# Kernel optimization log

Hardware: AMD Instinct MI355X
Metric: run time of the kernel (lower is better)

The kernel has to match this reference:

```python
import jax, jax.numpy as jnp
import numpy as np

SEQ_LEN = 4096
EMBED_DIM = 1024
NUM_HEADS = 16  # head_dim = 64


def setup_inputs() -> dict:
    key = jax.random.key(0)
    k0, k1, k2 = jax.random.split(key, 3)
    std = 0.02
    x = jax.random.normal(k0, (SEQ_LEN, EMBED_DIM), dtype=jnp.float32)
    # torch Linear convention: weight [out_features, in_features], y = x @ W.T + b
    W_qkv = jax.random.normal(k1, (3 * EMBED_DIM, EMBED_DIM), dtype=jnp.float32) * std
    b_qkv = jnp.zeros((3 * EMBED_DIM,), dtype=jnp.float32)
    W_out = jax.random.normal(k2, (EMBED_DIM, EMBED_DIM), dtype=jnp.float32) * std
    b_out = jnp.zeros((EMBED_DIM,), dtype=jnp.float32)
    return {"input": x, "W_qkv": W_qkv, "b_qkv": b_qkv, "W_out": W_out, "b_out": b_out}


def reference(input, W_qkv, b_qkv, W_out, b_out):
    S, E = input.shape
    H = NUM_HEADS
    Dh = E // H
    # fused QKV projection: [S, 3E]
    projected = input @ W_qkv.T + b_qkv
    q, k, v = jnp.split(projected, 3, axis=1)          # each [S, E]
    q = q.reshape(S, H, Dh)
    k = k.reshape(S, H, Dh)
    v = v.reshape(S, H, Dh)
    # unscaled attention (the original applies no 1/sqrt(d) scaling)
    scores = jnp.einsum('shd,thd->hst', q, k)          # [H, S, S] -- full matrix in HBM
    probs = jax.nn.softmax(scores, axis=-1)
    out = jnp.einsum('hst,thd->shd', probs, v)         # [S, H, Dh]
    out = out.reshape(S, E)
    return out @ W_out.T + b_out
```

## Files before the change

### kernel.cpp

```cpp
#include <hip/hip_runtime.h>

typedef unsigned short u16;
typedef short    bf16x8 __attribute__((ext_vector_type(8)));
typedef u16      u16x8  __attribute__((ext_vector_type(8)));
typedef u16      u16x4  __attribute__((ext_vector_type(4)));
typedef float    f32x4  __attribute__((ext_vector_type(4)));
typedef unsigned u32x2  __attribute__((ext_vector_type(2)));

__device__ __forceinline__ u16 f2bf(float f) {
  unsigned x = __float_as_uint(f);
  unsigned r = x + 0x7fffu + ((x >> 16) & 1u);
  return (u16)(r >> 16);
}
__device__ __forceinline__ float bf2f(u16 u) {
  return __uint_as_float(((unsigned)u) << 16);
}
__device__ __forceinline__ float exp2v(float x) {
  float r;
  asm("v_exp_f32 %0, %1" : "=v"(r) : "v"(x));
  return r;
}

__global__ __launch_bounds__(256) void cast_bf16(const float* __restrict__ src,
                                                 u16* __restrict__ dst) {
  int i = blockIdx.x * 256 + threadIdx.x;
  f32x4 v = ((const f32x4*)src)[i];
  u16x4 o;
  o[0] = f2bf(v[0]); o[1] = f2bf(v[1]); o[2] = f2bf(v[2]); o[3] = f2bf(v[3]);
  ((u16x4*)dst)[i] = o;
}

template<int N, int K, bool OUTF32, bool SCALEQ>
__global__ __launch_bounds__(256) void gemm_bt(const u16* __restrict__ A,
                                               const u16* __restrict__ B,
                                               const float* __restrict__ bias,
                                               void* __restrict__ Cout) {
  __shared__ __align__(16) u16 As[2][128 * 32];
  __shared__ __align__(16) u16 Bs[2][128 * 32];
  const int tid = threadIdx.x;
  const int flat = blockIdx.y * gridDim.x + blockIdx.x;
  const int q8 = (gridDim.x * gridDim.y) >> 3;
  const int sw = (flat & 7) * q8 + (flat >> 3);
  const int m0 = (sw / gridDim.x) * 128, n0 = (sw % gridDim.x) * 128;
  const int wave = tid >> 6, lane = tid & 63;
  const int c = lane & 15, g = lane >> 4;
  const int wm = (wave >> 1) * 64, wn = (wave & 1) * 64;
  f32x4 acc[4][4] = {};

  const int sr = wave * 16 + (lane >> 2);
  const int sc = (lane & 3) * 8;

  auto stage = [&](int buf, int k0) {
#pragma unroll
    for (int j = 0; j < 2; j++) {
      __builtin_amdgcn_global_load_lds(
        (const __attribute__((address_space(1))) void*)(A + (size_t)(m0 + j * 64 + sr) * K + k0 + sc),
        (__attribute__((address_space(3))) void*)&As[buf][(j * 64 + wave * 16) * 32], 16, 0, 0);
      __builtin_amdgcn_global_load_lds(
        (const __attribute__((address_space(1))) void*)(B + (size_t)(n0 + j * 64 + sr) * K + k0 + sc),
        (__attribute__((address_space(3))) void*)&Bs[buf][(j * 64 + wave * 16) * 32], 16, 0, 0);
    }
  };

  stage(0, 0);
  __syncthreads();

  const int nT = K / 32;
  for (int t = 0; t < nT; ++t) {
    const int buf = t & 1;
    if (t + 1 < nT) stage(buf ^ 1, (t + 1) * 32);
    bf16x8 af[4], bfr[4];
#pragma unroll
    for (int m = 0; m < 4; m++) af[m]  = *(const bf16x8*)&As[buf][(wm + m * 16 + c) * 32 + g * 8];
#pragma unroll
    for (int n = 0; n < 4; n++) bfr[n] = *(const bf16x8*)&Bs[buf][(wn + n * 16 + c) * 32 + g * 8];
#pragma unroll
    for (int m = 0; m < 4; m++)
#pragma unroll
      for (int n = 0; n < 4; n++)
        acc[m][n] = __builtin_amdgcn_mfma_f32_16x16x32_bf16(af[m], bfr[n], acc[m][n], 0, 0, 0);
    __syncthreads();
  }

  const float qscale = (SCALEQ && n0 < 1024) ? 1.44269504f : 1.0f;
#pragma unroll
  for (int n = 0; n < 4; n++) {
    float bv = bias[n0 + wn + n * 16 + c];
#pragma unroll
    for (int m = 0; m < 4; m++) {
#pragma unroll
      for (int r = 0; r < 4; r++) {
        float val = (acc[m][n][r] + bv) * qscale;
        int row = m0 + wm + m * 16 + g * 4 + r;
        int col = n0 + wn + n * 16 + c;
        if constexpr (OUTF32) ((float*)Cout)[(size_t)row * N + col] = val;
        else                  ((u16*)Cout)[(size_t)row * N + col] = f2bf(val);
      }
    }
  }
}

__global__ __launch_bounds__(256) void transpose_v(const u16* __restrict__ qkv,
                                                   u16* __restrict__ vt) {
  __shared__ u16 tile[64][64];
  int h  = blockIdx.x >> 6;
  int s0 = (blockIdx.x & 63) * 64;
  int t = threadIdx.x;
  int row = t >> 3, ch = t & 7;
#pragma unroll
  for (int rep = 0; rep < 2; rep++) {
    int r = rep * 32 + row;
    u16x8 v = *(const u16x8*)&qkv[(size_t)(s0 + r) * 3072 + 2048 + h * 64 + ch * 8];
    *(u16x8*)&tile[r][ch * 8] = v;
  }
  __syncthreads();
#pragma unroll
  for (int rep = 0; rep < 2; rep++) {
    int d = rep * 32 + row;
    u16x8 w;
#pragma unroll
    for (int j = 0; j < 8; j++) w[j] = tile[ch * 8 + j][d];
    *(u16x8*)&vt[(size_t)(h * 64 + d) * 4096 + s0 + ch * 8] = w;
  }
}

__global__ __launch_bounds__(256, 4) void attn_kernel(const u16* __restrict__ qkv,
                                                      const u16* __restrict__ vt,
                                                      u16* __restrict__ pb0,
                                                      u16* __restrict__ pb1,
                                                      float* __restrict__ lb0,
                                                      float* __restrict__ lb1) {
  const int bid = blockIdx.x;
  const int kk  = bid & 1;
  const int qt  = (bid >> 1) & 31;
  const int h   = bid >> 6;
  const int q0  = qt * 128;
  const int kbase = kk * 2048;
  const int tid = threadIdx.x;
  const int wave = tid >> 6, lane = tid & 63;
  const int c = lane & 15, g = lane >> 4;
  const int qw = q0 + wave * 32;

  __shared__ __align__(16) u16 kls[2][64 * 64];
  __shared__ __align__(16) u16 vls[2][64 * 64];
  __shared__ __align__(16) unsigned plds[4][16 * 32];
  unsigned* pw = plds[wave];
  const int pswz = (c & 7) << 2;

  const u16* Kg = qkv + 1024 + h * 64;
  const u16* Vg = vt + (size_t)h * 64 * 4096;

  const int srow = lane >> 3, sgr = lane & 7;
  const int gc = sgr ^ (srow & 7);
  const u16* kp = Kg + (size_t)(kbase + wave * 16 + srow) * 3072 + gc * 8;
  const u16* vp = Vg + (size_t)(wave * 16 + srow) * 4096 + kbase + gc * 8;

  auto stage = [&](int buf, const u16* kpp, const u16* vpp) {
#pragma unroll
    for (int j = 0; j < 2; j++) {
      __builtin_amdgcn_global_load_lds(
        (const __attribute__((address_space(1))) void*)(kpp + (size_t)j * 8 * 3072),
        (__attribute__((address_space(3))) void*)&kls[buf][(wave * 16 + j * 8) * 64], 16, 0, 0);
      __builtin_amdgcn_global_load_lds(
        (const __attribute__((address_space(1))) void*)(vpp + (size_t)j * 8 * 4096),
        (__attribute__((address_space(3))) void*)&vls[buf][(wave * 16 + j * 8) * 64], 16, 0, 0);
    }
  };

  bf16x8 qf[2][2];
#pragma unroll
  for (int qs = 0; qs < 2; qs++)
#pragma unroll
    for (int dc = 0; dc < 2; dc++)
      qf[qs][dc] = *(const bf16x8*)&qkv[(size_t)(qw + qs * 16 + c) * 3072 + h * 64 + dc * 32 + g * 8];

  bf16x8 ones;
#pragma unroll
  for (int j = 0; j < 8; j++) ones[j] = (short)0x3F80;

  f32x4 o0[4] = {}, o1[4] = {};
  f32x4 accl0 = {}, accl1 = {};
  const f32x4 minit = {-16.f, -16.f, -16.f, -16.f};

  auto softmax = [&](f32x4 (&st)[4]) {
#pragma unroll
    for (int ks = 0; ks < 4; ks++) {
      float p0 = exp2v(st[ks][0]), p1 = exp2v(st[ks][1]);
      float p2 = exp2v(st[ks][2]), p3 = exp2v(st[ks][3]);
      unsigned w0, w1;
      asm("v_cvt_pk_bf16_f32 %0, %1, %2" : "=v"(w0) : "v"(p0), "v"(p1));
      asm("v_cvt_pk_bf16_f32 %0, %1, %2" : "=v"(w1) : "v"(p2), "v"(p3));
      u32x2 w2 = {w0, w1};
      *(u32x2*)&pw[c * 32 + ((ks * 8 + g * 2) ^ pswz)] = w2;
    }
  };

  stage(0, kp, vp);
  kp += (size_t)64 * 3072; vp += 64;
  __syncthreads();

  for (int t = 0; t < 32; ++t) {
    const int buf = t & 1;
    if (t + 1 < 32) {
      stage(buf ^ 1, kp, vp);
      kp += (size_t)64 * 3072; vp += 64;
    }

    f32x4 st0[4], st1[4];
    __builtin_amdgcn_s_setprio(1);
#pragma unroll
    for (int ks = 0; ks < 4; ks++) {
      bf16x8 kf0 = *(const bf16x8*)&kls[buf][(ks * 16 + c) * 64 + ((g ^ (c & 7)) << 3)];
      bf16x8 kf1 = *(const bf16x8*)&kls[buf][(ks * 16 + c) * 64 + (((4 + g) ^ (c & 7)) << 3)];
      f32x4 s0 = __builtin_amdgcn_mfma_f32_16x16x32_bf16(kf0, qf[0][0], minit, 0, 0, 0);
      st0[ks]  = __builtin_amdgcn_mfma_f32_16x16x32_bf16(kf1, qf[0][1], s0, 0, 0, 0);
      f32x4 s1 = __builtin_amdgcn_mfma_f32_16x16x32_bf16(kf0, qf[1][0], minit, 0, 0, 0);
      st1[ks]  = __builtin_amdgcn_mfma_f32_16x16x32_bf16(kf1, qf[1][1], s1, 0, 0, 0);
    }
    __builtin_amdgcn_s_setprio(0);

    softmax(st0);
    bf16x8 pa0[2], pa1[2];
#pragma unroll
    for (int hh = 0; hh < 2; hh++)
      pa0[hh] = *(const bf16x8*)&pw[c * 32 + ((hh * 16 + g * 4) ^ pswz)];
    softmax(st1);
#pragma unroll
    for (int hh = 0; hh < 2; hh++)
      pa1[hh] = *(const bf16x8*)&pw[c * 32 + ((hh * 16 + g * 4) ^ pswz)];

    __builtin_amdgcn_s_setprio(1);
#pragma unroll
    for (int k2 = 0; k2 < 2; k2++) {
      accl0 = __builtin_amdgcn_mfma_f32_16x16x32_bf16(pa0[k2], ones, accl0, 0, 0, 0);
      accl1 = __builtin_amdgcn_mfma_f32_16x16x32_bf16(pa1[k2], ones, accl1, 0, 0, 0);
#pragma unroll
      for (int dt = 0; dt < 4; dt++) {
        bf16x8 vf = *(const bf16x8*)&vls[buf][(dt * 16 + c) * 64 + (((k2 * 4 + g) ^ (c & 7)) << 3)];
        o0[dt] = __builtin_amdgcn_mfma_f32_16x16x32_bf16(pa0[k2], vf, o0[dt], 0, 0, 0);
        o1[dt] = __builtin_amdgcn_mfma_f32_16x16x32_bf16(pa1[k2], vf, o1[dt], 0, 0, 0);
      }
    }
    __builtin_amdgcn_s_setprio(0);
    __syncthreads();
  }

  u16* pb = kk ? pb1 : pb0;
  float* lb = (kk ? lb1 : lb0) + h * 4096 + qw;
  u16* pq = pb + (size_t)qw * 1024 + h * 64;

#pragma unroll
  for (int r = 0; r < 4; r++) {
    int rl = g * 4 + r;
    float inv0 = 1.0f / accl0[r];
    float inv1 = 1.0f / accl1[r];
#pragma unroll
    for (int dt = 0; dt < 4; dt++) {
      pq[(size_t)rl * 1024 + dt * 16 + c]        = f2bf(o0[dt][r] * inv0);
      pq[(size_t)(16 + rl) * 1024 + dt * 16 + c] = f2bf(o1[dt][r] * inv1);
    }
    if (c == 0) {
      lb[rl]      = accl0[r];
      lb[16 + rl] = accl1[r];
    }
  }
}

__global__ __launch_bounds__(256) void combine_kernel(u16* __restrict__ pb0,
                                                      const u16* __restrict__ pb1,
                                                      const float* __restrict__ lb0,
                                                      const float* __restrict__ lb1) {
  int t = blockIdx.x * 256 + threadIdx.x;
  int q = t >> 7;
  int c8 = t & 127;
  int h = c8 >> 3;
  float A = lb0[h * 4096 + q];
  float B = lb1[h * 4096 + q];
  float inv = 1.0f / (A + B);
  float w0 = A * inv, w1 = B * inv;
  size_t off = (size_t)q * 1024 + c8 * 8;
  u16x8 x0 = *(const u16x8*)(pb0 + off);
  u16x8 x1 = *(const u16x8*)(pb1 + off);
  u16x8 o;
#pragma unroll
  for (int e = 0; e < 8; e++)
    o[e] = f2bf(bf2f(x0[e]) * w0 + bf2f(x1[e]) * w1);
  *(u16x8*)(pb0 + off) = o;
}

extern "C" void kernel_launch(void* const* d_in, const int* in_sizes, int n_in,
                              void* d_out, int out_size, void* d_ws, size_t ws_size,
                              hipStream_t stream) {
  const float* x    = (const float*)d_in[0];
  const float* Wqkv = (const float*)d_in[1];
  const float* bqkv = (const float*)d_in[2];
  const float* Wout = (const float*)d_in[3];
  const float* bout = (const float*)d_in[4];

  char* ws = (char*)d_ws;
  u16* xb    = (u16*)(ws);
  u16* wqkvb = (u16*)(ws + (size_t)8  * (1u << 20));
  u16* woutb = (u16*)(ws + (size_t)14 * (1u << 20));
  u16* qkvb  = (u16*)(ws + (size_t)16 * (1u << 20));
  u16* vtb   = (u16*)(ws + (size_t)40 * (1u << 20));
  u16* pb0   = (u16*)(ws + (size_t)48 * (1u << 20));
  char* dob = (char*)d_out;
  u16*   pb1 = (u16*)dob;
  float* lb0 = (float*)(dob + (size_t)8 * (1u << 20));
  float* lb1 = lb0 + 65536;

  cast_bf16<<<4096, 256, 0, stream>>>(x,    xb);
  cast_bf16<<<3072, 256, 0, stream>>>(Wqkv, wqkvb);
  cast_bf16<<<1024, 256, 0, stream>>>(Wout, woutb);

  gemm_bt<3072, 1024, false, true><<<dim3(24, 32), 256, 0, stream>>>(xb, wqkvb, bqkv, qkvb);

  transpose_v<<<1024, 256, 0, stream>>>(qkvb, vtb);

  attn_kernel<<<1024, 256, 0, stream>>>(qkvb, vtb, pb0, pb1, lb0, lb1);

  combine_kernel<<<2048, 256, 0, stream>>>(pb0, pb1, lb0, lb1);

  gemm_bt<1024, 1024, true, false><<<dim3(8, 32), 256, 0, stream>>>(pb0, woutb, bout, d_out);
}
```

Baseline: 176.8 us.

## Double attention query tile per wave to 64 rows for more K/V reuse

Each wave now processes 64 query rows (4 sub-tiles of 16) instead of 32, so each workgroup covers 256 queries and the grid halves to 512 blocks. K and V tiles staged in LDS are reused across twice as many queries, which halves global K/V traffic and LDS fragment loads per unit of work. In exchange, register pressure roughly doubles (launch bounds lowered to 2 waves-per-EU hint), which cuts occupancy, and 512 blocks may fill the 256 CUs less evenly.

Measured after the change: 172.4 us. 1.03x faster.

```diff
diff --git a/kernel.cpp b/kernel.cpp
--- a/kernel.cpp
+++ b/kernel.cpp
@@ -124,7 +124,7 @@
   }
 }
 
-__global__ __launch_bounds__(256, 4) void attn_kernel(const u16* __restrict__ qkv,
+__global__ __launch_bounds__(256, 2) void attn_kernel(const u16* __restrict__ qkv,
                                                       const u16* __restrict__ vt,
                                                       u16* __restrict__ pb0,
                                                       u16* __restrict__ pb1,
@@ -132,14 +132,14 @@
                                                       float* __restrict__ lb1) {
   const int bid = blockIdx.x;
   const int kk  = bid & 1;
-  const int qt  = (bid >> 1) & 31;
-  const int h   = bid >> 6;
-  const int q0  = qt * 128;
+  const int qt  = (bid >> 1) & 15;
+  const int h   = bid >> 5;
+  const int q0  = qt * 256;
   const int kbase = kk * 2048;
   const int tid = threadIdx.x;
   const int wave = tid >> 6, lane = tid & 63;
   const int c = lane & 15, g = lane >> 4;
-  const int qw = q0 + wave * 32;
+  const int qw = q0 + wave * 64;
 
   __shared__ __align__(16) u16 kls[2][64 * 64];
   __shared__ __align__(16) u16 vls[2][64 * 64];
@@ -167,9 +167,9 @@
     }
   };
 
-  bf16x8 qf[2][2];
-#pragma unroll
-  for (int qs = 0; qs < 2; qs++)
+  bf16x8 qf[4][2];
+#pragma unroll
+  for (int qs = 0; qs < 4; qs++)
 #pragma unroll
     for (int dc = 0; dc < 2; dc++)
       qf[qs][dc] = *(const bf16x8*)&qkv[(size_t)(qw + qs * 16 + c) * 3072 + h * 64 + dc * 32 + g * 8];
@@ -178,8 +178,8 @@
 #pragma unroll
   for (int j = 0; j < 8; j++) ones[j] = (short)0x3F80;
 
-  f32x4 o0[4] = {}, o1[4] = {};
-  f32x4 accl0 = {}, accl1 = {};
+  f32x4 o[4][4] = {};
+  f32x4 accl[4] = {};
   const f32x4 minit = {-16.f, -16.f, -16.f, -16.f};
 
   auto softmax = [&](f32x4 (&st)[4]) {
@@ -206,39 +206,41 @@
       kp += (size_t)64 * 3072; vp += 64;
     }
 
-    f32x4 st0[4], st1[4];
+    f32x4 st[4][4];
     __builtin_amdgcn_s_setprio(1);
 #pragma unroll
     for (int ks = 0; ks < 4; ks++) {
       bf16x8 kf0 = *(const bf16x8*)&kls[buf][(ks * 16 + c) * 64 + ((g ^ (c & 7)) << 3)];
       bf16x8 kf1 = *(const bf16x8*)&kls[buf][(ks * 16 + c) * 64 + (((4 + g) ^ (c & 7)) << 3)];
-      f32x4 s0 = __builtin_amdgcn_mfma_f32_16x16x32_bf16(kf0, qf[0][0], minit, 0, 0, 0);
-      st0[ks]  = __builtin_amdgcn_mfma_f32_16x16x32_bf16(kf1, qf[0][1], s0, 0, 0, 0);
-      f32x4 s1 = __builtin_amdgcn_mfma_f32_16x16x32_bf16(kf0, qf[1][0], minit, 0, 0, 0);
-      st1[ks]  = __builtin_amdgcn_mfma_f32_16x16x32_bf16(kf1, qf[1][1], s1, 0, 0, 0);
+#pragma unroll
+      for (int qs = 0; qs < 4; qs++) {
+        f32x4 s = __builtin_amdgcn_mfma_f32_16x16x32_bf16(kf0, qf[qs][0], minit, 0, 0, 0);
+        st[qs][ks] = __builtin_amdgcn_mfma_f32_16x16x32_bf16(kf1, qf[qs][1], s, 0, 0, 0);
+      }
     }
     __builtin_amdgcn_s_setprio(0);
 
-    softmax(st0);
-    bf16x8 pa0[2], pa1[2];
-#pragma unroll
-    for (int hh = 0; hh < 2; hh++)
-      pa0[hh] = *(const bf16x8*)&pw[c * 32 + ((hh * 16 + g * 4) ^ pswz)];
-    softmax(st1);
-#pragma unroll
-    for (int hh = 0; hh < 2; hh++)
-      pa1[hh] = *(const bf16x8*)&pw[c * 32 + ((hh * 16 + g * 4) ^ pswz)];
+    bf16x8 pa[4][2];
+#pragma unroll
+    for (int qs = 0; qs < 4; qs++) {
+      softmax(st[qs]);
+#pragma unroll
+      for (int hh = 0; hh < 2; hh++)
+        pa[qs][hh] = *(const bf16x8*)&pw[c * 32 + ((hh * 16 + g * 4) ^ pswz)];
+    }
 
     __builtin_amdgcn_s_setprio(1);
 #pragma unroll
     for (int k2 = 0; k2 < 2; k2++) {
-      accl0 = __builtin_amdgcn_mfma_f32_16x16x32_bf16(pa0[k2], ones, accl0, 0, 0, 0);
-      accl1 = __builtin_amdgcn_mfma_f32_16x16x32_bf16(pa1[k2], ones, accl1, 0, 0, 0);
+#pragma unroll
+      for (int qs = 0; qs < 4; qs++)
+        accl[qs] = __builtin_amdgcn_mfma_f32_16x16x32_bf16(pa[qs][k2], ones, accl[qs], 0, 0, 0);
 #pragma unroll
       for (int dt = 0; dt < 4; dt++) {
         bf16x8 vf = *(const bf16x8*)&vls[buf][(dt * 16 + c) * 64 + (((k2 * 4 + g) ^ (c & 7)) << 3)];
-        o0[dt] = __builtin_amdgcn_mfma_f32_16x16x32_bf16(pa0[k2], vf, o0[dt], 0, 0, 0);
-        o1[dt] = __builtin_amdgcn_mfma_f32_16x16x32_bf16(pa1[k2], vf, o1[dt], 0, 0, 0);
+#pragma unroll
+        for (int qs = 0; qs < 4; qs++)
+          o[qs][dt] = __builtin_amdgcn_mfma_f32_16x16x32_bf16(pa[qs][k2], vf, o[qs][dt], 0, 0, 0);
       }
     }
     __builtin_amdgcn_s_setprio(0);
@@ -250,18 +252,15 @@
   u16* pq = pb + (size_t)qw * 1024 + h * 64;
 
 #pragma unroll
-  for (int r = 0; r < 4; r++) {
-    int rl = g * 4 + r;
-    float inv0 = 1.0f / accl0[r];
-    float inv1 = 1.0f / accl1[r];
-#pragma unroll
-    for (int dt = 0; dt < 4; dt++) {
-      pq[(size_t)rl * 1024 + dt * 16 + c]        = f2bf(o0[dt][r] * inv0);
-      pq[(size_t)(16 + rl) * 1024 + dt * 16 + c] = f2bf(o1[dt][r] * inv1);
-    }
-    if (c == 0) {
-      lb[rl]      = accl0[r];
-      lb[16 + rl] = accl1[r];
+  for (int qs = 0; qs < 4; qs++) {
+#pragma unroll
+    for (int r = 0; r < 4; r++) {
+      int rl = g * 4 + r;
+      float inv = 1.0f / accl[qs][r];
+#pragma unroll
+      for (int dt = 0; dt < 4; dt++)
+        pq[(size_t)(qs * 16 + rl) * 1024 + dt * 16 + c] = f2bf(o[qs][dt][r] * inv);
+      if (c == 0) lb[qs * 16 + rl] = accl[qs][r];
     }
   }
 }
@@ -317,7 +316,7 @@
 
   transpose_v<<<1024, 256, 0, stream>>>(qkvb, vtb);
 
-  attn_kernel<<<1024, 256, 0, stream>>>(qkvb, vtb, pb0, pb1, lb0, lb1);
+  attn_kernel<<<512, 256, 0, stream>>>(qkvb, vtb, pb0, pb1, lb0, lb1);
 
   combine_kernel<<<2048, 256, 0, stream>>>(pb0, pb1, lb0, lb1);
 
```

## Fuse V transpose into QKV GEMM epilogue and merge cast kernels

Applied to the files above, without the earlier changes.

The three fp32-to-bf16 cast launches become one kernel that selects its source by block index. The separate V transpose kernel is removed. Instead, QKV GEMM blocks that cover the V columns transpose their tile through a swizzled LDS buffer and write V^T directly, skipping the normal V store. This saves two kernel launches and one read-write pass over V, at the cost of an extra LDS round trip and sync in the V-column blocks' epilogue.

Result: faster. 170.7 us (-3.4%).

```diff
diff --git a/kernel.cpp b/kernel.cpp
--- a/kernel.cpp
+++ b/kernel.cpp
@@ -21,22 +21,30 @@
   return r;
 }
 
-__global__ __launch_bounds__(256) void cast_bf16(const float* __restrict__ src,
-                                                 u16* __restrict__ dst) {
-  int i = blockIdx.x * 256 + threadIdx.x;
-  f32x4 v = ((const f32x4*)src)[i];
+__global__ __launch_bounds__(256) void cast3(const float* __restrict__ x,
+                                             const float* __restrict__ wq,
+                                             const float* __restrict__ wo,
+                                             u16* __restrict__ xb,
+                                             u16* __restrict__ wqb,
+                                             u16* __restrict__ wob) {
+  int b = blockIdx.x;
+  const float* s; u16* d; int i;
+  if (b < 4096)      { s = x;  d = xb;  i = b * 256 + threadIdx.x; }
+  else if (b < 7168) { s = wq; d = wqb; i = (b - 4096) * 256 + threadIdx.x; }
+  else               { s = wo; d = wob; i = (b - 7168) * 256 + threadIdx.x; }
+  f32x4 v = ((const f32x4*)s)[i];
   u16x4 o;
   o[0] = f2bf(v[0]); o[1] = f2bf(v[1]); o[2] = f2bf(v[2]); o[3] = f2bf(v[3]);
-  ((u16x4*)dst)[i] = o;
-}
-
-template<int N, int K, bool OUTF32, bool SCALEQ>
+  ((u16x4*)d)[i] = o;
+}
+
+template<int N, int K, bool OUTF32, bool SCALEQ, bool VSPLIT>
 __global__ __launch_bounds__(256) void gemm_bt(const u16* __restrict__ A,
                                                const u16* __restrict__ B,
                                                const float* __restrict__ bias,
-                                               void* __restrict__ Cout) {
-  __shared__ __align__(16) u16 As[2][128 * 32];
-  __shared__ __align__(16) u16 Bs[2][128 * 32];
+                                               void* __restrict__ Cout,
+                                               u16* __restrict__ vtout) {
+  __shared__ __align__(16) u16 smem[16384];
   const int tid = threadIdx.x;
   const int flat = blockIdx.y * gridDim.x + blockIdx.x;
   const int q8 = (gridDim.x * gridDim.y) >> 3;
@@ -55,10 +63,10 @@
     for (int j = 0; j < 2; j++) {
       __builtin_amdgcn_global_load_lds(
         (const __attribute__((address_space(1))) void*)(A + (size_t)(m0 + j * 64 + sr) * K + k0 + sc),
-        (__attribute__((address_space(3))) void*)&As[buf][(j * 64 + wave * 16) * 32], 16, 0, 0);
+        (__attribute__((address_space(3))) void*)&smem[buf * 4096 + (j * 64 + wave * 16) * 32], 16, 0, 0);
       __builtin_amdgcn_global_load_lds(
         (const __attribute__((address_space(1))) void*)(B + (size_t)(n0 + j * 64 + sr) * K + k0 + sc),
-        (__attribute__((address_space(3))) void*)&Bs[buf][(j * 64 + wave * 16) * 32], 16, 0, 0);
+        (__attribute__((address_space(3))) void*)&smem[8192 + buf * 4096 + (j * 64 + wave * 16) * 32], 16, 0, 0);
     }
   };
 
@@ -71,15 +79,45 @@
     if (t + 1 < nT) stage(buf ^ 1, (t + 1) * 32);
     bf16x8 af[4], bfr[4];
 #pragma unroll
-    for (int m = 0; m < 4; m++) af[m]  = *(const bf16x8*)&As[buf][(wm + m * 16 + c) * 32 + g * 8];
-#pragma unroll
-    for (int n = 0; n < 4; n++) bfr[n] = *(const bf16x8*)&Bs[buf][(wn + n * 16 + c) * 32 + g * 8];
+    for (int m = 0; m < 4; m++)
+      af[m]  = *(const bf16x8*)&smem[buf * 4096 + (wm + m * 16 + c) * 32 + g * 8];
+#pragma unroll
+    for (int n = 0; n < 4; n++)
+      bfr[n] = *(const bf16x8*)&smem[8192 + buf * 4096 + (wn + n * 16 + c) * 32 + g * 8];
 #pragma unroll
     for (int m = 0; m < 4; m++)
 #pragma unroll
       for (int n = 0; n < 4; n++)
         acc[m][n] = __builtin_amdgcn_mfma_f32_16x16x32_bf16(af[m], bfr[n], acc[m][n], 0, 0, 0);
     __syncthreads();
+  }
+
+  if (VSPLIT && n0 >= 2048) {
+#pragma unroll
+    for (int n = 0; n < 4; n++) {
+      float bv = bias[n0 + wn + n * 16 + c];
+#pragma unroll
+      for (int m = 0; m < 4; m++) {
+#pragma unroll
+        for (int r = 0; r < 4; r++) {
+          int nl = wn + n * 16 + c;
+          int ml = wm + m * 16 + g * 4 + r;
+          int Gs = (ml >> 3) ^ (nl & 15);
+          smem[nl * 128 + (Gs << 3) + (ml & 7)] = f2bf(acc[m][n][r] + bv);
+        }
+      }
+    }
+    __syncthreads();
+    const int nl = tid >> 1, half = tid & 1;
+    const int hd = n0 - 2048 + nl;
+    u16* dst = vtout + (size_t)hd * 4096 + m0 + half * 64;
+#pragma unroll
+    for (int Gj = 0; Gj < 8; Gj++) {
+      int G = half * 8 + Gj;
+      u16x8 v = *(const u16x8*)&smem[nl * 128 + ((G ^ (nl & 15)) << 3)];
+      *(u16x8*)(dst + Gj * 8) = v;
+    }
+    return;
   }
 
   const float qscale = (SCALEQ && n0 < 1024) ? 1.44269504f : 1.0f;
@@ -97,30 +135,6 @@
         else                  ((u16*)Cout)[(size_t)row * N + col] = f2bf(val);
       }
     }
-  }
-}
-
-__global__ __launch_bounds__(256) void transpose_v(const u16* __restrict__ qkv,
-                                                   u16* __restrict__ vt) {
-  __shared__ u16 tile[64][64];
-  int h  = blockIdx.x >> 6;
-  int s0 = (blockIdx.x & 63) * 64;
-  int t = threadIdx.x;
-  int row = t >> 3, ch = t & 7;
-#pragma unroll
-  for (int rep = 0; rep < 2; rep++) {
-    int r = rep * 32 + row;
-    u16x8 v = *(const u16x8*)&qkv[(size_t)(s0 + r) * 3072 + 2048 + h * 64 + ch * 8];
-    *(u16x8*)&tile[r][ch * 8] = v;
-  }
-  __syncthreads();
-#pragma unroll
-  for (int rep = 0; rep < 2; rep++) {
-    int d = rep * 32 + row;
-    u16x8 w;
-#pragma unroll
-    for (int j = 0; j < 8; j++) w[j] = tile[ch * 8 + j][d];
-    *(u16x8*)&vt[(size_t)(h * 64 + d) * 4096 + s0 + ch * 8] = w;
   }
 }
 
@@ -309,17 +323,15 @@
   float* lb0 = (float*)(dob + (size_t)8 * (1u << 20));
   float* lb1 = lb0 + 65536;
 
-  cast_bf16<<<4096, 256, 0, stream>>>(x,    xb);
-  cast_bf16<<<3072, 256, 0, stream>>>(Wqkv, wqkvb);
-  cast_bf16<<<1024, 256, 0, stream>>>(Wout, woutb);
-
-  gemm_bt<3072, 1024, false, true><<<dim3(24, 32), 256, 0, stream>>>(xb, wqkvb, bqkv, qkvb);
-
-  transpose_v<<<1024, 256, 0, stream>>>(qkvb, vtb);
+  cast3<<<8192, 256, 0, stream>>>(x, Wqkv, Wout, xb, wqkvb, woutb);
+
+  gemm_bt<3072, 1024, false, true, true><<<dim3(24, 32), 256, 0, stream>>>(
+      xb, wqkvb, bqkv, qkvb, vtb);
 
   attn_kernel<<<1024, 256, 0, stream>>>(qkvb, vtb, pb0, pb1, lb0, lb1);
 
   combine_kernel<<<2048, 256, 0, stream>>>(pb0, pb1, lb0, lb1);
 
-  gemm_bt<1024, 1024, true, false><<<dim3(8, 32), 256, 0, stream>>>(pb0, woutb, bout, d_out);
-}
+  gemm_bt<1024, 1024, true, false, false><<<dim3(8, 32), 256, 0, stream>>>(
+      pb0, woutb, bout, d_out, nullptr);
+}
```
